# Optimization experiments

Hardware: AMD Instinct MI355X
Metric: run time of the kernel (lower is better)

## Reference

```python
import jax, jax.numpy as jnp
import numpy as np

HIDDEN_DIM = 64
MEMORY_SLOTS = 8
SEQ_LEN = 24
VOCAB_SIZE = 64
B = 262144


def setup_inputs() -> dict:
    key = jax.random.key(0)
    ks = jax.random.split(key, 7)
    return {
        "seqs": jax.random.randint(ks[0], (B, SEQ_LEN), 0, VOCAB_SIZE, dtype=jnp.int64) if jax.config.jax_enable_x64 else jax.random.randint(ks[0], (B, SEQ_LEN), 0, VOCAB_SIZE, dtype=jnp.int32),
        "query_tok": jax.random.randint(ks[1], (B,), 0, VOCAB_SIZE, dtype=jnp.int32),
        "embed_W": jax.random.normal(ks[2], (VOCAB_SIZE + 2, HIDDEN_DIM), dtype=jnp.float32),
        "W1": jax.random.normal(ks[3], (HIDDEN_DIM, 2 * HIDDEN_DIM), dtype=jnp.float32) * 0.08,
        "b1": jax.random.normal(ks[4], (HIDDEN_DIM,), dtype=jnp.float32) * 0.02,
        "W2": jax.random.normal(ks[5], (VOCAB_SIZE, HIDDEN_DIM), dtype=jnp.float32) * 0.12,
        "b2": jax.random.normal(ks[6], (VOCAB_SIZE,), dtype=jnp.float32) * 0.02,
    }


def reference(seqs, query_tok, embed_W, W1, b1, W2, b2):
    # FIFO of size MEMORY_SLOTS over tokens t in [0, SEQ_LEN-1):
    # mem_summary depends only on the last MEMORY_SLOTS of those tokens.
    mem_toks = seqs[:, SEQ_LEN - 1 - MEMORY_SLOTS : SEQ_LEN - 1]      # [B, M]
    mem_summary = jnp.mean(embed_W[mem_toks], axis=1)                 # [B, H]
    q_emb = embed_W[query_tok]                                        # [B, H]
    x = jnp.concatenate([q_emb, mem_summary], axis=-1)               # [B, 2H]
    h = jax.nn.relu(x @ W1.T + b1)                                    # [B, H]
    logits = h @ W2.T + b2                                            # [B, V]
    return logits
```

## Files before the change

kernel.cpp:

```cpp
#include <hip/hip_runtime.h>
#include <hip/hip_bf16.h>


#define TSTRIDE 68
#define T2_OFF  (64 * TSTRIDE)
#define LDS_WORDS (2 * 64 * TSTRIDE)

typedef __attribute__((ext_vector_type(4))) float f32x4;
typedef __attribute__((ext_vector_type(8))) short bf16x8;

__device__ __forceinline__ unsigned pkbf2(float a, float b) {
  float2 f2; f2.x = a; f2.y = b;
  __hip_bfloat162 h = __float22bfloat162_rn(f2);
  union { __hip_bfloat162 h2; unsigned u; } cv; cv.h2 = h;
  return cv.u;
}

__global__ void prep_kernel(const float* __restrict__ embed,
                            const float* __restrict__ W1,
                            const float* __restrict__ b1,
                            float* __restrict__ T) {
  const int t    = blockIdx.x & 63;
  const int half = blockIdx.x >> 6;
  const int j    = threadIdx.x;
  const float* wrow = W1 + j * 128 + half * 64;
  const float* erow = embed + t * 64;
  float acc = 0.f;
#pragma unroll
  for (int k = 0; k < 64; ++k) acc += wrow[k] * erow[k];
  const float outv = half ? acc * 0.125f : acc + b1[j];
  T[half * T2_OFF + t * TSTRIDE + j] = outv;
}

__global__ __launch_bounds__(256, 4) void lru_kernel(
    const int*   __restrict__ seqs,
    const int*   __restrict__ qtok,
    const float* __restrict__ W2,
    const float* __restrict__ b2,
    const float* __restrict__ T,
    float*       __restrict__ out) {
  __shared__ __align__(16) float lds[LDS_WORDS];
  const int tid = threadIdx.x;

  {
    const f32x4* src = (const f32x4*)T;
    f32x4*       dst = (f32x4*)lds;
#pragma unroll 1
    for (int i = tid; i < LDS_WORDS / 4; i += 256) dst[i] = src[i];
  }

  const int lane = tid & 63;
  const int wv   = tid >> 6;
  const int qd   = lane >> 4;
  const int l15  = lane & 15;

  bf16x8 bfr[4][2];
  f32x4  binit[4];
#pragma unroll
  for (int nt = 0; nt < 4; ++nt) {
    const float* wr = W2 + (nt * 16 + l15) * 64 + qd * 8;
#pragma unroll
    for (int ks = 0; ks < 2; ++ks) {
      f32x4 w0 = *(const f32x4*)(wr + ks * 32);
      f32x4 w1 = *(const f32x4*)(wr + ks * 32 + 4);
      union { bf16x8 s; unsigned u[4]; } ub;
      ub.u[0] = pkbf2(w0[0], w0[1]);
      ub.u[1] = pkbf2(w0[2], w0[3]);
      ub.u[2] = pkbf2(w1[0], w1[1]);
      ub.u[3] = pkbf2(w1[2], w1[3]);
      bfr[nt][ks] = ub.s;
    }
    const float bb = b2[nt * 16 + l15];
    binit[nt][0] = bb; binit[nt][1] = bb; binit[nt][2] = bb; binit[nt][3] = bb;
  }
  __syncthreads();

  const int base = blockIdx.x * 256 + wv * 64;
#pragma unroll 1
  for (int it = 0; it < 4; ++it) {
    const int b0   = base + it * 16;
    const int elem = b0 + l15;

    const int* srow = seqs + elem * 24;
    const int4 c0 = *(const int4*)(srow + 12);
    const int4 c1 = *(const int4*)(srow + 16);
    const int4 c2 = *(const int4*)(srow + 20);
    const int  qt = qtok[elem];
    const int tk[8] = {c0.w, c1.x, c1.y, c1.z, c1.w, c2.x, c2.y, c2.z};

    const float* r1 = lds + qt * TSTRIDE + qd * 8;
    f32x4 a0 = *(const f32x4*)(r1);
    f32x4 a1 = *(const f32x4*)(r1 + 4);
    f32x4 a2 = *(const f32x4*)(r1 + 32);
    f32x4 a3 = *(const f32x4*)(r1 + 36);
#pragma unroll
    for (int s = 0; s < 8; ++s) {
      const float* r2 = lds + T2_OFF + tk[s] * TSTRIDE + qd * 8;
      a0 += *(const f32x4*)(r2);
      a1 += *(const f32x4*)(r2 + 4);
      a2 += *(const f32x4*)(r2 + 32);
      a3 += *(const f32x4*)(r2 + 36);
    }
#pragma unroll
    for (int i = 0; i < 4; ++i) {
      a0[i] = fmaxf(a0[i], 0.f);
      a1[i] = fmaxf(a1[i], 0.f);
      a2[i] = fmaxf(a2[i], 0.f);
      a3[i] = fmaxf(a3[i], 0.f);
    }
    union { bf16x8 s; unsigned u[4]; } ua, ub2;
    ua.u[0]  = pkbf2(a0[0], a0[1]);
    ua.u[1]  = pkbf2(a0[2], a0[3]);
    ua.u[2]  = pkbf2(a1[0], a1[1]);
    ua.u[3]  = pkbf2(a1[2], a1[3]);
    ub2.u[0] = pkbf2(a2[0], a2[1]);
    ub2.u[1] = pkbf2(a2[2], a2[3]);
    ub2.u[2] = pkbf2(a3[0], a3[1]);
    ub2.u[3] = pkbf2(a3[2], a3[3]);
    const bf16x8 afA = ua.s, afB = ub2.s;

#pragma unroll
    for (int nt = 0; nt < 4; ++nt) {
      f32x4 acc = binit[nt];
      acc = __builtin_amdgcn_mfma_f32_16x16x32_bf16(afA, bfr[nt][0], acc, 0, 0, 0);
      acc = __builtin_amdgcn_mfma_f32_16x16x32_bf16(afB, bfr[nt][1], acc, 0, 0, 0);
      float* op = out + (size_t)(b0 + qd * 4) * 64 + nt * 16 + l15;
#pragma unroll
      for (int r = 0; r < 4; ++r) op[(size_t)r * 64] = acc[r];
    }
  }
}

extern "C" void kernel_launch(void* const* d_in, const int* in_sizes, int n_in,
                              void* d_out, int out_size, void* d_ws, size_t ws_size,
                              hipStream_t stream) {
  const int*   seqs  = (const int*)d_in[0];
  const int*   qtokp = (const int*)d_in[1];
  const float* embed = (const float*)d_in[2];
  const float* W1    = (const float*)d_in[3];
  const float* b1    = (const float*)d_in[4];
  const float* W2    = (const float*)d_in[5];
  const float* b2    = (const float*)d_in[6];
  float*       outp  = (float*)d_out;
  float*       T     = (float*)d_ws;

  prep_kernel<<<dim3(128), dim3(64), 0, stream>>>(embed, W1, b1, T);
  lru_kernel<<<dim3(1024), dim3(256), 0, stream>>>(seqs, qtokp, W2, b2, T, outp);
}
```

Measured before the change: 117.6 us.

## Store precomputed W1 projection tables as bf16 and double grid size

```diff
diff --git a/kernel.cpp b/kernel.cpp
--- a/kernel.cpp
+++ b/kernel.cpp
@@ -2,24 +2,26 @@
 #include <hip/hip_bf16.h>
 
 
-#define TSTRIDE 68
-#define T2_OFF  (64 * TSTRIDE)
-#define LDS_WORDS (2 * 64 * TSTRIDE)
+#define RSTRIDE_W 36
+#define T2_OFF_W  (64 * RSTRIDE_W)
+#define LDS_DW    (2 * 64 * RSTRIDE_W)
 
 typedef __attribute__((ext_vector_type(4))) float f32x4;
 typedef __attribute__((ext_vector_type(8))) short bf16x8;
 
+__device__ __forceinline__ unsigned short f2bf(float x) {
+  union { float f; unsigned u; } c; c.f = x;
+  unsigned u = c.u + 0x7fffu + ((c.u >> 16) & 1u);
+  return (unsigned short)(u >> 16);
+}
 __device__ __forceinline__ unsigned pkbf2(float a, float b) {
-  float2 f2; f2.x = a; f2.y = b;
-  __hip_bfloat162 h = __float22bfloat162_rn(f2);
-  union { __hip_bfloat162 h2; unsigned u; } cv; cv.h2 = h;
-  return cv.u;
+  return (unsigned)f2bf(a) | ((unsigned)f2bf(b) << 16);
 }
 
 __global__ void prep_kernel(const float* __restrict__ embed,
                             const float* __restrict__ W1,
                             const float* __restrict__ b1,
-                            float* __restrict__ T) {
+                            unsigned short* __restrict__ T) {
   const int t    = blockIdx.x & 63;
   const int half = blockIdx.x >> 6;
   const int j    = threadIdx.x;
@@ -29,24 +31,25 @@
 #pragma unroll
   for (int k = 0; k < 64; ++k) acc += wrow[k] * erow[k];
   const float outv = half ? acc * 0.125f : acc + b1[j];
-  T[half * T2_OFF + t * TSTRIDE + j] = outv;
+  T[half * (64 * 2 * RSTRIDE_W) + t * (2 * RSTRIDE_W) + j] = f2bf(outv);
 }
 
 __global__ __launch_bounds__(256, 4) void lru_kernel(
-    const int*   __restrict__ seqs,
-    const int*   __restrict__ qtok,
-    const float* __restrict__ W2,
-    const float* __restrict__ b2,
-    const float* __restrict__ T,
-    float*       __restrict__ out) {
-  __shared__ __align__(16) float lds[LDS_WORDS];
+    const int*      __restrict__ seqs,
+    const int*      __restrict__ qtok,
+    const float*    __restrict__ W2,
+    const float*    __restrict__ b2,
+    const unsigned* __restrict__ T,
+    float*          __restrict__ out) {
+  __shared__ __align__(16) unsigned lds[LDS_DW];
   const int tid = threadIdx.x;
 
   {
-    const f32x4* src = (const f32x4*)T;
-    f32x4*       dst = (f32x4*)lds;
-#pragma unroll 1
-    for (int i = tid; i < LDS_WORDS / 4; i += 256) dst[i] = src[i];
+    const uint4* src = (const uint4*)T;
+    uint4*       dst = (uint4*)lds;
+#pragma unroll
+    for (int r = 0; r < 4; ++r) dst[tid + r * 256] = src[tid + r * 256];
+    if (tid < 128) dst[tid + 1024] = src[tid + 1024];
   }
 
   const int lane = tid & 63;
@@ -55,7 +58,7 @@
   const int l15  = lane & 15;
 
   bf16x8 bfr[4][2];
-  f32x4  binit[4];
+  float  bb[4];
 #pragma unroll
   for (int nt = 0; nt < 4; ++nt) {
     const float* wr = W2 + (nt * 16 + l15) * 64 + qd * 8;
@@ -70,14 +73,13 @@
       ub.u[3] = pkbf2(w1[2], w1[3]);
       bfr[nt][ks] = ub.s;
     }
-    const float bb = b2[nt * 16 + l15];
-    binit[nt][0] = bb; binit[nt][1] = bb; binit[nt][2] = bb; binit[nt][3] = bb;
+    bb[nt] = b2[nt * 16 + l15];
   }
   __syncthreads();
 
-  const int base = blockIdx.x * 256 + wv * 64;
-#pragma unroll 1
-  for (int it = 0; it < 4; ++it) {
+  const int base = blockIdx.x * 128 + wv * 32;
+#pragma unroll
+  for (int it = 0; it < 2; ++it) {
     const int b0   = base + it * 16;
     const int elem = b0 + l15;
 
@@ -88,40 +90,45 @@
     const int  qt = qtok[elem];
     const int tk[8] = {c0.w, c1.x, c1.y, c1.z, c1.w, c2.x, c2.y, c2.z};
 
-    const float* r1 = lds + qt * TSTRIDE + qd * 8;
-    f32x4 a0 = *(const f32x4*)(r1);
-    f32x4 a1 = *(const f32x4*)(r1 + 4);
-    f32x4 a2 = *(const f32x4*)(r1 + 32);
-    f32x4 a3 = *(const f32x4*)(r1 + 36);
+    float alo[8], ahi[8];
+    {
+      const unsigned* r1 = lds + qt * RSTRIDE_W + qd * 4;
+      uint4 d0 = *(const uint4*)(r1);
+      uint4 d1 = *(const uint4*)(r1 + 16);
+#pragma unroll
+      for (int i = 0; i < 4; ++i) {
+        alo[i]     = __uint_as_float(d0[i] << 16);
+        ahi[i]     = __uint_as_float(d0[i] & 0xffff0000u);
+        alo[4 + i] = __uint_as_float(d1[i] << 16);
+        ahi[4 + i] = __uint_as_float(d1[i] & 0xffff0000u);
+      }
+    }
 #pragma unroll
     for (int s = 0; s < 8; ++s) {
-      const float* r2 = lds + T2_OFF + tk[s] * TSTRIDE + qd * 8;
-      a0 += *(const f32x4*)(r2);
-      a1 += *(const f32x4*)(r2 + 4);
-      a2 += *(const f32x4*)(r2 + 32);
-      a3 += *(const f32x4*)(r2 + 36);
+      const unsigned* r2 = lds + T2_OFF_W + tk[s] * RSTRIDE_W + qd * 4;
+      uint4 d0 = *(const uint4*)(r2);
+      uint4 d1 = *(const uint4*)(r2 + 16);
+#pragma unroll
+      for (int i = 0; i < 4; ++i) {
+        alo[i]     += __uint_as_float(d0[i] << 16);
+        ahi[i]     += __uint_as_float(d0[i] & 0xffff0000u);
+        alo[4 + i] += __uint_as_float(d1[i] << 16);
+        ahi[4 + i] += __uint_as_float(d1[i] & 0xffff0000u);
+      }
     }
+
+    union { bf16x8 s; unsigned u[4]; } ua, ub2;
 #pragma unroll
     for (int i = 0; i < 4; ++i) {
-      a0[i] = fmaxf(a0[i], 0.f);
-      a1[i] = fmaxf(a1[i], 0.f);
-      a2[i] = fmaxf(a2[i], 0.f);
-      a3[i] = fmaxf(a3[i], 0.f);
+      ua.u[i]  = pkbf2(fmaxf(alo[i], 0.f),     fmaxf(ahi[i], 0.f));
+      ub2.u[i] = pkbf2(fmaxf(alo[4 + i], 0.f), fmaxf(ahi[4 + i], 0.f));
     }
-    union { bf16x8 s; unsigned u[4]; } ua, ub2;
-    ua.u[0]  = pkbf2(a0[0], a0[1]);
-    ua.u[1]  = pkbf2(a0[2], a0[3]);
-    ua.u[2]  = pkbf2(a1[0], a1[1]);
-    ua.u[3]  = pkbf2(a1[2], a1[3]);
-    ub2.u[0] = pkbf2(a2[0], a2[1]);
-    ub2.u[1] = pkbf2(a2[2], a2[3]);
-    ub2.u[2] = pkbf2(a3[0], a3[1]);
-    ub2.u[3] = pkbf2(a3[2], a3[3]);
     const bf16x8 afA = ua.s, afB = ub2.s;
 
 #pragma unroll
     for (int nt = 0; nt < 4; ++nt) {
-      f32x4 acc = binit[nt];
+      f32x4 acc;
+      acc[0] = bb[nt]; acc[1] = bb[nt]; acc[2] = bb[nt]; acc[3] = bb[nt];
       acc = __builtin_amdgcn_mfma_f32_16x16x32_bf16(afA, bfr[nt][0], acc, 0, 0, 0);
       acc = __builtin_amdgcn_mfma_f32_16x16x32_bf16(afB, bfr[nt][1], acc, 0, 0, 0);
       float* op = out + (size_t)(b0 + qd * 4) * 64 + nt * 16 + l15;
@@ -142,8 +149,9 @@
   const float* W2    = (const float*)d_in[5];
   const float* b2    = (const float*)d_in[6];
   float*       outp  = (float*)d_out;
-  float*       T     = (float*)d_ws;
 
-  prep_kernel<<<dim3(128), dim3(64), 0, stream>>>(embed, W1, b1, T);
-  lru_kernel<<<dim3(1024), dim3(256), 0, stream>>>(seqs, qtokp, W2, b2, T, outp);
+  prep_kernel<<<dim3(128), dim3(64), 0, stream>>>(embed, W1, b1,
+                                                  (unsigned short*)d_ws);
+  lru_kernel<<<dim3(2048), dim3(256), 0, stream>>>(seqs, qtokp, W2, b2,
+                                                   (const unsigned*)d_ws, outp);
 }
```

Result: no change. 117.0 us (-0.5%).
